# Optimization experiments

Hardware: AMD Instinct MI355X
Metric: run time of the kernel (lower is better)

Reference implementation:

```python
import jax, jax.numpy as jnp
import numpy as np

E = 1024      # embed_dim
H = 16        # num_heads
HD = E // H   # head_dim = 64


def setup_inputs() -> dict:
    key = jax.random.key(0)
    ks = jax.random.split(key, 8)
    T, B, S = 1024, 4, 1024
    return {
        "query": jax.random.normal(ks[0], (T, B, E), jnp.float32),
        "key": jax.random.normal(ks[1], (S, B, E), jnp.float32),
        "value": jax.random.normal(ks[2], (S, B, E), jnp.float32),
        "attn_mask": jax.random.normal(ks[3], (T, S), jnp.float32),
        "key_padding_mask": jax.random.randint(ks[4], (B, S), 0, 2, jnp.int32),
        "in_proj_weight": jax.random.normal(ks[5], (3 * E, E), jnp.float32) * 0.02,
        "in_proj_bias": jnp.zeros((3 * E,), jnp.float32),
        "out_w": jax.random.normal(ks[6], (E, E), jnp.float32) * 0.02,
        "out_b": jnp.zeros((E,), jnp.float32),
    }


def reference(query, key, value, attn_mask, key_padding_mask,
              in_proj_weight, in_proj_bias, out_w, out_b):
    T, B, _ = query.shape
    S = key.shape[0]
    w_q, w_k, w_v = jnp.split(in_proj_weight, 3, axis=0)   # each [E, E]
    b_q, b_k, b_v = jnp.split(in_proj_bias, 3, axis=0)
    q = query @ w_q.T + b_q                                # [T, B, E]
    k = key @ w_k.T + b_k                                  # [S, B, E]
    v = value @ w_v.T + b_v                                # [S, B, E]
    # [len, B, E] -> [B*H, len, HD]
    q = q.reshape(T, B * H, HD).transpose(1, 0, 2) / jnp.sqrt(jnp.float32(HD))
    k = k.reshape(S, B * H, HD).transpose(1, 0, 2)
    v = v.reshape(S, B * H, HD).transpose(1, 0, 2)
    scores = jnp.einsum('bth,bsh->bts', q, k)              # [B*H, T, S]
    scores = scores + attn_mask[None]                      # float additive mask
    pad = key_padding_mask.astype(bool)                    # [B, S]
    pad = jnp.broadcast_to(pad[:, None, None, :], (B, H, 1, S)).reshape(B * H, 1, S)
    scores = jnp.where(pad, -jnp.inf, scores)
    weights = jax.nn.softmax(scores, axis=-1)              # dropout p=0 -> identity
    out = jnp.einsum('bts,bsh->bth', weights, v)           # [B*H, T, HD]
    out = out.transpose(1, 0, 2).reshape(T, B, E)
    out = out @ out_w.T + out_b
    weights_avg = weights.reshape(B, H, T, S).mean(axis=1) # sum/H == mean
    return out, weights_avg
```

## Files before the change

kernel.cpp:

```cpp
#include <hip/hip_runtime.h>
#include <stdint.h>

typedef short bf16x8 __attribute__((ext_vector_type(8)));
typedef float f32x4  __attribute__((ext_vector_type(4)));

#define LOG2E_F 1.4426950408889634f
#define QSCALE_F 0.1803368801111204f

__device__ __forceinline__ unsigned short f2bf(float f) {
    unsigned int u = __float_as_uint(f);
    return (unsigned short)((u + 0x7FFFu + ((u >> 16) & 1u)) >> 16);
}

__device__ __forceinline__ unsigned short f2bfu(float f) {
    return (unsigned short)((__float_as_uint(f) + 0x8000u) >> 16);
}

__device__ __forceinline__ uint4 pack8(float4 a, float4 b) {
    union { unsigned short us[8]; uint4 v; } p;
    p.us[0] = f2bf(a.x); p.us[1] = f2bf(a.y); p.us[2] = f2bf(a.z); p.us[3] = f2bf(a.w);
    p.us[4] = f2bf(b.x); p.us[5] = f2bf(b.y); p.us[6] = f2bf(b.z); p.us[7] = f2bf(b.w);
    return p.v;
}

__global__ __launch_bounds__(256)
void cvt_kernel(const float* __restrict__ q, const float* __restrict__ k,
                const float* __restrict__ v, const float* __restrict__ w,
                const float* __restrict__ ow,
                uint4* __restrict__ Xb, uint4* __restrict__ Wb, uint4* __restrict__ OWb)
{
    const unsigned g = blockIdx.x * 256 + threadIdx.x;
    const float* src;
    uint4* dst;
    if (g < 1572864u) {
        dst = Xb + g;
        if (g < 524288u)        src = q + (size_t)g * 8;
        else if (g < 1048576u)  src = k + (size_t)(g - 524288u) * 8;
        else                    src = v + (size_t)(g - 1048576u) * 8;
    } else if (g < 1966080u) {
        src = w + (size_t)(g - 1572864u) * 8;
        dst = Wb + (g - 1572864u);
    } else {
        src = ow + (size_t)(g - 1966080u) * 8;
        dst = OWb + (g - 1966080u);
    }
    float4 a = *(const float4*)src;
    float4 b = *(const float4*)(src + 4);
    *dst = pack8(a, b);
}

__global__ __launch_bounds__(256)
void mtr_kernel(const float* __restrict__ m, float* __restrict__ mt)
{
    __shared__ float tile[64][65];
    const int bt = (blockIdx.x & 15) << 6;
    const int bs = (blockIdx.x >> 4) << 6;
    const int tx = threadIdx.x & 63;
    const int ty = threadIdx.x >> 6;
#pragma unroll
    for (int i = 0; i < 64; i += 4)
        tile[ty + i][tx] = m[(size_t)(bt + ty + i) * 1024 + bs + tx];
    __syncthreads();
#pragma unroll
    for (int i = 0; i < 64; i += 4) {
        const int s = bs + ty + i;
        mt[(size_t)(s >> 2) * 4096 + (bt + tx) * 4 + (s & 3)] = tile[tx][ty + i];
    }
}

__global__ __launch_bounds__(256)
void qkv_proj_kernel(const unsigned short* __restrict__ Xb, const unsigned short* __restrict__ Wb,
                     const float* __restrict__ bias,
                     unsigned short* __restrict__ Qb, unsigned short* __restrict__ Kb,
                     unsigned short* __restrict__ Vtb)
{
    const int z = blockIdx.z;
    const int j   = blockIdx.x;
    const int xcd = j & 7, idx = j >> 3;
    const int row0 = ((xcd << 2) + (idx >> 3)) * 128;
    const int col0 = (idx & 7) * 128;
    const int wofs = z << 10;

    const unsigned short* A = Xb + (size_t)z * 4194304;
    const unsigned short* B = Wb;

    __shared__ __align__(16) unsigned short As[128 * 72];
    __shared__ __align__(16) unsigned short Bs[128 * 72];

    const int tid  = threadIdx.x;
    const int lane = tid & 63;
    const int wv   = tid >> 6;
    const int wr   = wv >> 1, wc = wv & 1;

    const f32x4 zero4 = {0.f, 0.f, 0.f, 0.f};
    f32x4 acc[4][4];
#pragma unroll
    for (int m = 0; m < 4; ++m)
#pragma unroll
        for (int n = 0; n < 4; ++n) acc[m][n] = zero4;

    const int srow = tid >> 1;
    const int scol = (tid & 1) << 5;
    const int arow = wr * 64 + (lane & 15);
    const int brow = wc * 64 + (lane & 15);
    const int kof  = (lane >> 4) << 3;

    const unsigned short* pa = A + (size_t)(row0 + srow) * 1024 + scol;
    const unsigned short* pb = B + (size_t)(wofs + col0 + srow) * 1024 + scol;
    uint4 ra0 = *(const uint4*)(pa + 0),  ra1 = *(const uint4*)(pa + 8);
    uint4 ra2 = *(const uint4*)(pa + 16), ra3 = *(const uint4*)(pa + 24);
    uint4 rb0 = *(const uint4*)(pb + 0),  rb1 = *(const uint4*)(pb + 8);
    uint4 rb2 = *(const uint4*)(pb + 16), rb3 = *(const uint4*)(pb + 24);

    for (int k0 = 0; k0 < 1024; k0 += 64) {
        __syncthreads();
        *(uint4*)&As[srow * 72 + scol]      = ra0;
        *(uint4*)&As[srow * 72 + scol + 8]  = ra1;
        *(uint4*)&As[srow * 72 + scol + 16] = ra2;
        *(uint4*)&As[srow * 72 + scol + 24] = ra3;
        *(uint4*)&Bs[srow * 72 + scol]      = rb0;
        *(uint4*)&Bs[srow * 72 + scol + 8]  = rb1;
        *(uint4*)&Bs[srow * 72 + scol + 16] = rb2;
        *(uint4*)&Bs[srow * 72 + scol + 24] = rb3;
        __syncthreads();

        if (k0 < 960) {
            pa = A + (size_t)(row0 + srow) * 1024 + k0 + 64 + scol;
            pb = B + (size_t)(wofs + col0 + srow) * 1024 + k0 + 64 + scol;
            ra0 = *(const uint4*)(pa + 0);  ra1 = *(const uint4*)(pa + 8);
            ra2 = *(const uint4*)(pa + 16); ra3 = *(const uint4*)(pa + 24);
            rb0 = *(const uint4*)(pb + 0);  rb1 = *(const uint4*)(pb + 8);
            rb2 = *(const uint4*)(pb + 16); rb3 = *(const uint4*)(pb + 24);
        }

#pragma unroll
        for (int kk = 0; kk < 2; ++kk) {
            bf16x8 af[4], bfr[4];
#pragma unroll
            for (int m = 0; m < 4; ++m)
                af[m] = *(const bf16x8*)&As[(arow + m * 16) * 72 + kk * 32 + kof];
#pragma unroll
            for (int n = 0; n < 4; ++n)
                bfr[n] = *(const bf16x8*)&Bs[(brow + n * 16) * 72 + kk * 32 + kof];
#pragma unroll
            for (int m = 0; m < 4; ++m)
#pragma unroll
                for (int n = 0; n < 4; ++n)
                    acc[m][n] = __builtin_amdgcn_mfma_f32_16x16x32_bf16(af[m], bfr[n], acc[m][n], 0, 0, 0);
        }
    }

    const int ccol = lane & 15;
    const int crow = (lane >> 4) << 2;
#pragma unroll
    for (int n = 0; n < 4; ++n) {
        const int gc   = col0 + wc * 64 + n * 16 + ccol;
        const float bv = bias[wofs + gc];
        const int head = gc >> 6, d = gc & 63;
#pragma unroll
        for (int m = 0; m < 4; ++m) {
#pragma unroll
            for (int r = 0; r < 4; ++r) {
                const int gr = row0 + wr * 64 + m * 16 + crow + r;
                const int t  = gr >> 2, b = gr & 3;
                const int bh = (b << 4) + head;
                float vv = acc[m][n][r] + bv;
                if (z == 0)      Qb [((size_t)bh << 16) + ((size_t)t << 6) + d]  = f2bf(vv * QSCALE_F);
                else if (z == 1) Kb [((size_t)bh << 16) + ((size_t)t << 6) + d]  = f2bf(vv);
                else             Vtb[((size_t)bh << 16) + ((size_t)d << 10) + t] = f2bf(vv);
            }
        }
    }
}

__global__ __launch_bounds__(512)
void flash_kernel(const unsigned short* __restrict__ Qb, const unsigned short* __restrict__ Kb,
                  const unsigned short* __restrict__ Vtb, const float* __restrict__ maskT,
                  const int* __restrict__ padmask,
                  float* __restrict__ rl_buf, unsigned short* __restrict__ attn_out)
{
    const int j   = blockIdx.x;
    const int xcd = j & 7, idx = j >> 3;
    const int bh  = xcd * 8 + (idx >> 3);
    const int t0  = (idx & 7) << 7;
    const int b   = bh >> 4, h = bh & 15;

    __shared__ __align__(16) unsigned short Ks[2][2][64 * 72];
    __shared__ __align__(16) unsigned short Vs[2][2][64 * 72];

    const int tid  = threadIdx.x;
    const int lane = tid & 63;
    const int wv   = tid >> 6;
    const int kof  = (lane >> 4) << 3;
    const int c16  = lane & 15;
    const int g4   = (lane >> 4) << 2;

    const unsigned short* Qbase = Qb  + ((size_t)bh << 16);
    const unsigned short* Kbase = Kb  + ((size_t)bh << 16);
    const unsigned short* Vbase = Vtb + ((size_t)bh << 16);

    bf16x8 qf[2];
#pragma unroll
    for (int kk = 0; kk < 2; ++kk)
        qf[kk] = *(const bf16x8*)(Qbase + ((size_t)(t0 + wv * 16 + c16) << 6) + kk * 32 + kof);

    const bf16x8 ones = {16256, 16256, 16256, 16256, 16256, 16256, 16256, 16256};

    const f32x4 zero4 = {0.f, 0.f, 0.f, 0.f};
    f32x4 acco[4];
#pragma unroll
    for (int nd = 0; nd < 4; ++nd) acco[nd] = zero4;
    f32x4 acc_l = zero4;

    const int srow_st = tid >> 3;
    const int scol_st = (tid & 7) << 3;

    const int bb  = scol_st & 31;
    const int hh  = scol_st & 32;
    const int cL  = hh + ((bb & 15) >> 2) * 8 + (bb >> 4) * 4;
    const int bb4 = bb + 4;
    const int cH  = hh + ((bb4 & 15) >> 2) * 8 + (bb4 >> 4) * 4;

    const int tr2 = t0 + wv * 16 + c16;

    const unsigned short* kp = Kbase + ((size_t)srow_st << 6) + scol_st;
    const unsigned short* vp = Vbase + ((size_t)srow_st << 10) + scol_st;
    uint4 kA = *(const uint4*)kp;
    uint4 kB = *(const uint4*)(kp + 4096);
    uint4 vA = *(const uint4*)vp;
    uint4 vB = *(const uint4*)(vp + 64);

    {
        *(uint4*)&Ks[0][0][srow_st * 72 + scol_st] = kA;
        *(uint4*)&Ks[0][1][srow_st * 72 + scol_st] = kB;
        uint2 lo, hi;
        lo.x = vA.x; lo.y = vA.y; hi.x = vA.z; hi.y = vA.w;
        *(uint2*)&Vs[0][0][srow_st * 72 + cL] = lo;
        *(uint2*)&Vs[0][0][srow_st * 72 + cH] = hi;
        lo.x = vB.x; lo.y = vB.y; hi.x = vB.z; hi.y = vB.w;
        *(uint2*)&Vs[0][1][srow_st * 72 + cL] = lo;
        *(uint2*)&Vs[0][1][srow_st * 72 + cH] = hi;
    }
    kp = Kbase + ((size_t)(128 + srow_st) << 6) + scol_st;
    vp = Vbase + ((size_t)srow_st << 10) + 128 + scol_st;
    kA = *(const uint4*)kp;
    kB = *(const uint4*)(kp + 4096);
    vA = *(const uint4*)vp;
    vB = *(const uint4*)(vp + 64);
    __syncthreads();

    for (int rd = 0; rd < 8; ++rd) {
        const int cur = rd & 1;
        const int s0  = rd << 7;

        if (rd < 7) {
            *(uint4*)&Ks[cur ^ 1][0][srow_st * 72 + scol_st] = kA;
            *(uint4*)&Ks[cur ^ 1][1][srow_st * 72 + scol_st] = kB;
            uint2 lo, hi;
            lo.x = vA.x; lo.y = vA.y; hi.x = vA.z; hi.y = vA.w;
            *(uint2*)&Vs[cur ^ 1][0][srow_st * 72 + cL] = lo;
            *(uint2*)&Vs[cur ^ 1][0][srow_st * 72 + cH] = hi;
            lo.x = vB.x; lo.y = vB.y; hi.x = vB.z; hi.y = vB.w;
            *(uint2*)&Vs[cur ^ 1][1][srow_st * 72 + cL] = lo;
            *(uint2*)&Vs[cur ^ 1][1][srow_st * 72 + cH] = hi;
        }
        if (rd < 6) {
            const int sn = s0 + 256;
            kp = Kbase + ((size_t)(sn + srow_st) << 6) + scol_st;
            vp = Vbase + ((size_t)srow_st << 10) + sn + scol_st;
            kA = *(const uint4*)kp;
            kB = *(const uint4*)(kp + 4096);
            vA = *(const uint4*)vp;
            vB = *(const uint4*)(vp + 64);
        }

        f32x4 accsA[4], accsB[4];
#pragma unroll
        for (int n = 0; n < 4; ++n) { accsA[n] = zero4; accsB[n] = zero4; }
        __builtin_amdgcn_s_setprio(1);
#pragma unroll
        for (int n = 0; n < 4; ++n) {
            bf16x8 kfA0 = *(const bf16x8*)&Ks[cur][0][(n * 16 + c16) * 72 + kof];
            bf16x8 kfA1 = *(const bf16x8*)&Ks[cur][0][(n * 16 + c16) * 72 + 32 + kof];
            accsA[n] = __builtin_amdgcn_mfma_f32_16x16x32_bf16(kfA0, qf[0], accsA[n], 0, 0, 0);
            accsA[n] = __builtin_amdgcn_mfma_f32_16x16x32_bf16(kfA1, qf[1], accsA[n], 0, 0, 0);
            bf16x8 kfB0 = *(const bf16x8*)&Ks[cur][1][(n * 16 + c16) * 72 + kof];
            bf16x8 kfB1 = *(const bf16x8*)&Ks[cur][1][(n * 16 + c16) * 72 + 32 + kof];
            accsB[n] = __builtin_amdgcn_mfma_f32_16x16x32_bf16(kfB0, qf[0], accsB[n], 0, 0, 0);
            accsB[n] = __builtin_amdgcn_mfma_f32_16x16x32_bf16(kfB1, qf[1], accsB[n], 0, 0, 0);
        }
        __builtin_amdgcn_s_setprio(0);

#pragma unroll
        for (int tile = 0; tile < 2; ++tile) {
            const int s0t = s0 + tile * 64;
            f32x4* accs = tile ? accsB : accsA;

            float4 mk[4];
            int4 pd[4];
#pragma unroll
            for (int n = 0; n < 4; ++n) {
                const int srow = s0t + n * 16 + g4;
                pd[n] = *(const int4*)(padmask + (b << 10) + srow);
                mk[n] = *(const float4*)(maskT + (size_t)(srow >> 2) * 4096 + tr2 * 4);
            }

            union { unsigned short us[16]; bf16x8 v[2]; } pk;
#pragma unroll
            for (int n = 0; n < 4; ++n) {
                float x0 = fmaf(mk[n].x, LOG2E_F, accs[n][0]);
                float x1 = fmaf(mk[n].y, LOG2E_F, accs[n][1]);
                float x2 = fmaf(mk[n].z, LOG2E_F, accs[n][2]);
                float x3 = fmaf(mk[n].w, LOG2E_F, accs[n][3]);
                if (pd[n].x) x0 = -1e30f;
                if (pd[n].y) x1 = -1e30f;
                if (pd[n].z) x2 = -1e30f;
                if (pd[n].w) x3 = -1e30f;
                pk.us[n * 4 + 0] = f2bfu(__builtin_amdgcn_exp2f(x0));
                pk.us[n * 4 + 1] = f2bfu(__builtin_amdgcn_exp2f(x1));
                pk.us[n * 4 + 2] = f2bfu(__builtin_amdgcn_exp2f(x2));
                pk.us[n * 4 + 3] = f2bfu(__builtin_amdgcn_exp2f(x3));
            }

            __builtin_amdgcn_s_setprio(1);
#pragma unroll
            for (int hhh = 0; hhh < 2; ++hhh) {
                bf16x8 pf = pk.v[hhh];
#pragma unroll
                for (int nd = 0; nd < 4; ++nd) {
                    bf16x8 vf = *(const bf16x8*)&Vs[cur][tile][(nd * 16 + c16) * 72 + hhh * 32 + kof];
                    acco[nd] = __builtin_amdgcn_mfma_f32_16x16x32_bf16(pf, vf, acco[nd], 0, 0, 0);
                }
                acc_l = __builtin_amdgcn_mfma_f32_16x16x32_bf16(pf, ones, acc_l, 0, 0, 0);
            }
            __builtin_amdgcn_s_setprio(0);
        }

        if (rd < 7) __syncthreads();
    }

#pragma unroll
    for (int r = 0; r < 4; ++r) {
        const int t = t0 + wv * 16 + g4 + r;
        const float rl = 1.0f / acc_l[r];
        if (c16 == 0)
            rl_buf[(bh << 10) + t] = rl;
#pragma unroll
        for (int nd = 0; nd < 4; ++nd) {
            const int d = nd * 16 + c16;
            attn_out[((size_t)t * 4 + b) * 1024 + h * 64 + d] = f2bf(acco[nd][r] * rl);
        }
    }
}

__global__ __launch_bounds__(256)
void wavg_kernel(const unsigned short* __restrict__ Qb, const unsigned short* __restrict__ Kb,
                 const float* __restrict__ attn_mask, const int* __restrict__ padmask,
                 const float* __restrict__ rl_buf, float* __restrict__ wout)
{
    const int j   = blockIdx.x;
    const int xcd = j & 7;
    const int b   = xcd >> 1;
    const int rr  = ((j >> 3) << 1) + (xcd & 1);
    const int t0  = (rr >> 4) << 6;
    const int s0  = (rr & 15) << 6;

    __shared__ __align__(16) unsigned short Qs[2][64 * 72];
    __shared__ __align__(16) unsigned short Ks2[2][64 * 72];

    const int tid  = threadIdx.x;
    const int lane = tid & 63;
    const int wv   = tid >> 6;
    const int wr   = wv >> 1, wc = wv & 1;
    const int kof  = (lane >> 4) << 3;
    const int srow_st = tid >> 2;
    const int scol_st = (tid & 3) << 4;

    const int t_base = t0 + wr * 32 + ((lane >> 4) << 2);
    const int s_base = s0 + wc * 32 + (lane & 15);

    int pad2[2];
#pragma unroll
    for (int nn = 0; nn < 2; ++nn) pad2[nn] = padmask[(b << 10) + s_base + nn * 16];

    float maskv[2][2][4];
#pragma unroll
    for (int mm = 0; mm < 2; ++mm)
#pragma unroll
        for (int r = 0; r < 4; ++r)
#pragma unroll
            for (int nn = 0; nn < 2; ++nn)
                maskv[mm][nn][r] = attn_mask[(size_t)(t_base + mm * 16 + r) * 1024 + s_base + nn * 16] * LOG2E_F;

    float wsum[2][2][4];
#pragma unroll
    for (int mm = 0; mm < 2; ++mm)
#pragma unroll
        for (int nn = 0; nn < 2; ++nn)
#pragma unroll
            for (int r = 0; r < 4; ++r) wsum[mm][nn][r] = 0.f;

    const unsigned short* qsrc = Qb + ((size_t)(t0 + srow_st) << 6) + scol_st;
    const unsigned short* ksrc = Kb + ((size_t)(s0 + srow_st) << 6) + scol_st;
    const size_t bh0 = (size_t)(b << 4) << 16;

    uint4 q0 = *(const uint4*)(qsrc + bh0);
    uint4 q1 = *(const uint4*)(qsrc + bh0 + 8);
    uint4 k0 = *(const uint4*)(ksrc + bh0);
    uint4 k1 = *(const uint4*)(ksrc + bh0 + 8);
    *(uint4*)&Qs[0][srow_st * 72 + scol_st]      = q0;
    *(uint4*)&Qs[0][srow_st * 72 + scol_st + 8]  = q1;
    *(uint4*)&Ks2[0][srow_st * 72 + scol_st]     = k0;
    *(uint4*)&Ks2[0][srow_st * 72 + scol_st + 8] = k1;
    q0 = *(const uint4*)(qsrc + bh0 + 65536);
    q1 = *(const uint4*)(qsrc + bh0 + 65536 + 8);
    k0 = *(const uint4*)(ksrc + bh0 + 65536);
    k1 = *(const uint4*)(ksrc + bh0 + 65536 + 8);
    __syncthreads();

#pragma unroll 2
    for (int h = 0; h < 16; ++h) {
        const int cur = h & 1;
        const int bh  = (b << 4) + h;

        if (h < 15) {
            *(uint4*)&Qs[cur ^ 1][srow_st * 72 + scol_st]      = q0;
            *(uint4*)&Qs[cur ^ 1][srow_st * 72 + scol_st + 8]  = q1;
            *(uint4*)&Ks2[cur ^ 1][srow_st * 72 + scol_st]     = k0;
            *(uint4*)&Ks2[cur ^ 1][srow_st * 72 + scol_st + 8] = k1;
        }
        if (h < 14) {
            const size_t of = bh0 + (size_t)(h + 2) * 65536;
            q0 = *(const uint4*)(qsrc + of);
            q1 = *(const uint4*)(qsrc + of + 8);
            k0 = *(const uint4*)(ksrc + of);
            k1 = *(const uint4*)(ksrc + of + 8);
        }

        float rlv[2][4];
#pragma unroll
        for (int mm = 0; mm < 2; ++mm)
#pragma unroll
            for (int r = 0; r < 4; ++r)
                rlv[mm][r] = rl_buf[(bh << 10) + t_base + mm * 16 + r];

        const f32x4 zero4 = {0.f, 0.f, 0.f, 0.f};
        f32x4 accs[2][2];
#pragma unroll
        for (int mm = 0; mm < 2; ++mm)
#pragma unroll
            for (int nn = 0; nn < 2; ++nn) accs[mm][nn] = zero4;
#pragma unroll
        for (int nn = 0; nn < 2; ++nn) {
            bf16x8 kf0 = *(const bf16x8*)&Ks2[cur][(wc * 32 + nn * 16 + (lane & 15)) * 72 + kof];
            bf16x8 kf1 = *(const bf16x8*)&Ks2[cur][(wc * 32 + nn * 16 + (lane & 15)) * 72 + 32 + kof];
#pragma unroll
            for (int mm = 0; mm < 2; ++mm) {
                bf16x8 qf0 = *(const bf16x8*)&Qs[cur][(wr * 32 + mm * 16 + (lane & 15)) * 72 + kof];
                bf16x8 qf1 = *(const bf16x8*)&Qs[cur][(wr * 32 + mm * 16 + (lane & 15)) * 72 + 32 + kof];
                accs[mm][nn] = __builtin_amdgcn_mfma_f32_16x16x32_bf16(qf0, kf0, accs[mm][nn], 0, 0, 0);
                accs[mm][nn] = __builtin_amdgcn_mfma_f32_16x16x32_bf16(qf1, kf1, accs[mm][nn], 0, 0, 0);
            }
        }
#pragma unroll
        for (int mm = 0; mm < 2; ++mm)
#pragma unroll
            for (int nn = 0; nn < 2; ++nn)
#pragma unroll
                for (int r = 0; r < 4; ++r)
                    if (!pad2[nn]) {
                        float x = accs[mm][nn][r] + maskv[mm][nn][r];
                        wsum[mm][nn][r] += __builtin_amdgcn_exp2f(x) * rlv[mm][r];
                    }

        if (h < 15) __syncthreads();
    }

#pragma unroll
    for (int mm = 0; mm < 2; ++mm)
#pragma unroll
        for (int nn = 0; nn < 2; ++nn)
#pragma unroll
            for (int r = 0; r < 4; ++r)
                wout[((size_t)b << 20) + (size_t)(t_base + mm * 16 + r) * 1024 + s_base + nn * 16]
                    = wsum[mm][nn][r] * 0.0625f;
}

__global__ __launch_bounds__(256)
void out_proj_kernel(const unsigned short* __restrict__ A, const unsigned short* __restrict__ Wb,
                     const float* __restrict__ bias, float* __restrict__ out)
{
    const int j   = blockIdx.x;
    const int xcd = j & 7, idx = j >> 3;
    const int row0 = ((xcd << 2) + (idx >> 3)) * 128;
    const int col0 = (idx & 7) * 128;

    __shared__ __align__(16) unsigned short As[128 * 72];
    __shared__ __align__(16) unsigned short Bs[128 * 72];

    const int tid  = threadIdx.x;
    const int lane = tid & 63;
    const int wv   = tid >> 6;
    const int wr   = wv >> 1, wc = wv & 1;

    const f32x4 zero4 = {0.f, 0.f, 0.f, 0.f};
    f32x4 acc[4][4];
#pragma unroll
    for (int m = 0; m < 4; ++m)
#pragma unroll
        for (int n = 0; n < 4; ++n) acc[m][n] = zero4;

    const int srow = tid >> 1;
    const int scol = (tid & 1) << 5;
    const int arow = wr * 64 + (lane & 15);
    const int brow = wc * 64 + (lane & 15);
    const int kof  = (lane >> 4) << 3;

    const unsigned short* pa = A  + (size_t)(row0 + srow) * 1024 + scol;
    const unsigned short* pb = Wb + (size_t)(col0 + srow) * 1024 + scol;
    uint4 ra0 = *(const uint4*)(pa + 0),  ra1 = *(const uint4*)(pa + 8);
    uint4 ra2 = *(const uint4*)(pa + 16), ra3 = *(const uint4*)(pa + 24);
    uint4 rb0 = *(const uint4*)(pb + 0),  rb1 = *(const uint4*)(pb + 8);
    uint4 rb2 = *(const uint4*)(pb + 16), rb3 = *(const uint4*)(pb + 24);

    for (int k0 = 0; k0 < 1024; k0 += 64) {
        __syncthreads();
        *(uint4*)&As[srow * 72 + scol]      = ra0;
        *(uint4*)&As[srow * 72 + scol + 8]  = ra1;
        *(uint4*)&As[srow * 72 + scol + 16] = ra2;
        *(uint4*)&As[srow * 72 + scol + 24] = ra3;
        *(uint4*)&Bs[srow * 72 + scol]      = rb0;
        *(uint4*)&Bs[srow * 72 + scol + 8]  = rb1;
        *(uint4*)&Bs[srow * 72 + scol + 16] = rb2;
        *(uint4*)&Bs[srow * 72 + scol + 24] = rb3;
        __syncthreads();

        if (k0 < 960) {
            pa = A  + (size_t)(row0 + srow) * 1024 + k0 + 64 + scol;
            pb = Wb + (size_t)(col0 + srow) * 1024 + k0 + 64 + scol;
            ra0 = *(const uint4*)(pa + 0);  ra1 = *(const uint4*)(pa + 8);
            ra2 = *(const uint4*)(pa + 16); ra3 = *(const uint4*)(pa + 24);
            rb0 = *(const uint4*)(pb + 0);  rb1 = *(const uint4*)(pb + 8);
            rb2 = *(const uint4*)(pb + 16); rb3 = *(const uint4*)(pb + 24);
        }

#pragma unroll
        for (int kk = 0; kk < 2; ++kk) {
            bf16x8 af[4], bfr[4];
#pragma unroll
            for (int m = 0; m < 4; ++m)
                af[m] = *(const bf16x8*)&As[(arow + m * 16) * 72 + kk * 32 + kof];
#pragma unroll
            for (int n = 0; n < 4; ++n)
                bfr[n] = *(const bf16x8*)&Bs[(brow + n * 16) * 72 + kk * 32 + kof];
#pragma unroll
            for (int m = 0; m < 4; ++m)
#pragma unroll
                for (int n = 0; n < 4; ++n)
                    acc[m][n] = __builtin_amdgcn_mfma_f32_16x16x32_bf16(af[m], bfr[n], acc[m][n], 0, 0, 0);
        }
    }

    const int ccol = lane & 15;
    const int crow = (lane >> 4) << 2;
#pragma unroll
    for (int n = 0; n < 4; ++n) {
        const int gc   = col0 + wc * 64 + n * 16 + ccol;
        const float bv = bias[gc];
#pragma unroll
        for (int m = 0; m < 4; ++m) {
#pragma unroll
            for (int r = 0; r < 4; ++r) {
                const int gr = row0 + wr * 64 + m * 16 + crow + r;
                out[(size_t)gr * 1024 + gc] = acc[m][n][r] + bv;
            }
        }
    }
}

extern "C" void kernel_launch(void* const* d_in, const int* in_sizes, int n_in,
                              void* d_out, int out_size, void* d_ws, size_t ws_size,
                              hipStream_t stream)
{
    const float* query     = (const float*)d_in[0];
    const float* key       = (const float*)d_in[1];
    const float* value     = (const float*)d_in[2];
    const float* attn_mask = (const float*)d_in[3];
    const int*   padmask   = (const int*)  d_in[4];
    const float* in_proj_w = (const float*)d_in[5];
    const float* in_proj_b = (const float*)d_in[6];
    const float* out_w     = (const float*)d_in[7];
    const float* out_b     = (const float*)d_in[8];

    float* out  = (float*)d_out;
    float* wavg = out + 4194304;

    char* ws = (char*)d_ws;
    unsigned short* Qb     = (unsigned short*)(ws);
    unsigned short* Kb     = (unsigned short*)(ws + 8388608);
    unsigned short* Vtb    = (unsigned short*)(ws + 16777216);
    unsigned short* Xb     = (unsigned short*)(ws + 25165824);
    unsigned short* attn_o = (unsigned short*)(ws + 25165824);
    float*          maskT  = (float*)(ws + 33554432);
    unsigned short* Wb     = (unsigned short*)(ws + 50331648);
    unsigned short* OWb    = (unsigned short*)(ws + 56623104);
    float*          rl_buf = (float*)(ws + 58720256);

    cvt_kernel<<<dim3(8192), 256, 0, stream>>>(query, key, value, in_proj_w, out_w,
                                               (uint4*)Xb, (uint4*)Wb, (uint4*)OWb);
    qkv_proj_kernel<<<dim3(256, 1, 3), 256, 0, stream>>>(Xb, Wb, in_proj_b, Qb, Kb, Vtb);
    mtr_kernel<<<dim3(256), 256, 0, stream>>>(attn_mask, maskT);
    flash_kernel<<<dim3(512), 512, 0, stream>>>(Qb, Kb, Vtb, maskT, padmask,
                                                rl_buf, attn_o);
    wavg_kernel<<<dim3(1024), 256, 0, stream>>>(Qb, Kb, attn_mask, padmask,
                                                rl_buf, wavg);
    out_proj_kernel<<<dim3(256), 256, 0, stream>>>(attn_o, OWb, out_b, out);
}
```

Baseline: 154.7 us.

## Load GEMM tiles directly into LDS via global_load_lds in projection kernels

```diff
diff --git a/kernel.cpp b/kernel.cpp
--- a/kernel.cpp
+++ b/kernel.cpp
@@ -21,6 +21,12 @@
     p.us[0] = f2bf(a.x); p.us[1] = f2bf(a.y); p.us[2] = f2bf(a.z); p.us[3] = f2bf(a.w);
     p.us[4] = f2bf(b.x); p.us[5] = f2bf(b.y); p.us[6] = f2bf(b.z); p.us[7] = f2bf(b.w);
     return p.v;
+}
+
+__device__ __forceinline__ void gload_lds16(const unsigned short* g, unsigned short* l) {
+    __builtin_amdgcn_global_load_lds(
+        (const __attribute__((address_space(1))) void*)g,
+        (__attribute__((address_space(3))) void*)l, 16, 0, 0);
 }
 
 __global__ __launch_bounds__(256)
@@ -84,13 +90,15 @@
     const unsigned short* A = Xb + (size_t)z * 4194304;
     const unsigned short* B = Wb;
 
-    __shared__ __align__(16) unsigned short As[128 * 72];
-    __shared__ __align__(16) unsigned short Bs[128 * 72];
+    __shared__ __align__(16) unsigned short As[128 * 32];
+    __shared__ __align__(16) unsigned short Bs[128 * 32];
 
     const int tid  = threadIdx.x;
     const int lane = tid & 63;
     const int wv   = tid >> 6;
     const int wr   = wv >> 1, wc = wv & 1;
+    const int c16  = lane & 15;
+    const int kof  = (lane >> 4) << 3;
 
     const f32x4 zero4 = {0.f, 0.f, 0.f, 0.f};
     f32x4 acc[4][4];
@@ -99,58 +107,37 @@
 #pragma unroll
         for (int n = 0; n < 4; ++n) acc[m][n] = zero4;
 
-    const int srow = tid >> 1;
-    const int scol = (tid & 1) << 5;
-    const int arow = wr * 64 + (lane & 15);
-    const int brow = wc * 64 + (lane & 15);
-    const int kof  = (lane >> 4) << 3;
-
-    const unsigned short* pa = A + (size_t)(row0 + srow) * 1024 + scol;
-    const unsigned short* pb = B + (size_t)(wofs + col0 + srow) * 1024 + scol;
-    uint4 ra0 = *(const uint4*)(pa + 0),  ra1 = *(const uint4*)(pa + 8);
-    uint4 ra2 = *(const uint4*)(pa + 16), ra3 = *(const uint4*)(pa + 24);
-    uint4 rb0 = *(const uint4*)(pb + 0),  rb1 = *(const uint4*)(pb + 8);
-    uint4 rb2 = *(const uint4*)(pb + 16), rb3 = *(const uint4*)(pb + 24);
-
-    for (int k0 = 0; k0 < 1024; k0 += 64) {
+    const unsigned short* gA = A + (size_t)(row0 + wv * 16 + (lane >> 2)) * 1024 + ((lane & 3) << 3);
+    const unsigned short* gB = B + (size_t)(wofs + col0 + wv * 16 + (lane >> 2)) * 1024 + ((lane & 3) << 3);
+    unsigned short* lA = As + tid * 8;
+    unsigned short* lB = Bs + tid * 8;
+
+    const int arow = wr * 64 + c16;
+    const int brow = wc * 64 + c16;
+
+    for (int k0 = 0; k0 < 1024; k0 += 32) {
         __syncthreads();
-        *(uint4*)&As[srow * 72 + scol]      = ra0;
-        *(uint4*)&As[srow * 72 + scol + 8]  = ra1;
-        *(uint4*)&As[srow * 72 + scol + 16] = ra2;
-        *(uint4*)&As[srow * 72 + scol + 24] = ra3;
-        *(uint4*)&Bs[srow * 72 + scol]      = rb0;
-        *(uint4*)&Bs[srow * 72 + scol + 8]  = rb1;
-        *(uint4*)&Bs[srow * 72 + scol + 16] = rb2;
-        *(uint4*)&Bs[srow * 72 + scol + 24] = rb3;
+        gload_lds16(gA + k0,         lA);
+        gload_lds16(gA + k0 + 65536, lA + 2048);
+        gload_lds16(gB + k0,         lB);
+        gload_lds16(gB + k0 + 65536, lB + 2048);
         __syncthreads();
 
-        if (k0 < 960) {
-            pa = A + (size_t)(row0 + srow) * 1024 + k0 + 64 + scol;
-            pb = B + (size_t)(wofs + col0 + srow) * 1024 + k0 + 64 + scol;
-            ra0 = *(const uint4*)(pa + 0);  ra1 = *(const uint4*)(pa + 8);
-            ra2 = *(const uint4*)(pa + 16); ra3 = *(const uint4*)(pa + 24);
-            rb0 = *(const uint4*)(pb + 0);  rb1 = *(const uint4*)(pb + 8);
-            rb2 = *(const uint4*)(pb + 16); rb3 = *(const uint4*)(pb + 24);
-        }
-
-#pragma unroll
-        for (int kk = 0; kk < 2; ++kk) {
-            bf16x8 af[4], bfr[4];
-#pragma unroll
-            for (int m = 0; m < 4; ++m)
-                af[m] = *(const bf16x8*)&As[(arow + m * 16) * 72 + kk * 32 + kof];
+        bf16x8 af[4], bfr[4];
+#pragma unroll
+        for (int m = 0; m < 4; ++m)
+            af[m] = *(const bf16x8*)&As[(arow + m * 16) * 32 + kof];
+#pragma unroll
+        for (int n = 0; n < 4; ++n)
+            bfr[n] = *(const bf16x8*)&Bs[(brow + n * 16) * 32 + kof];
+#pragma unroll
+        for (int m = 0; m < 4; ++m)
 #pragma unroll
             for (int n = 0; n < 4; ++n)
-                bfr[n] = *(const bf16x8*)&Bs[(brow + n * 16) * 72 + kk * 32 + kof];
-#pragma unroll
-            for (int m = 0; m < 4; ++m)
-#pragma unroll
-                for (int n = 0; n < 4; ++n)
-                    acc[m][n] = __builtin_amdgcn_mfma_f32_16x16x32_bf16(af[m], bfr[n], acc[m][n], 0, 0, 0);
-        }
-    }
-
-    const int ccol = lane & 15;
+                acc[m][n] = __builtin_amdgcn_mfma_f32_16x16x32_bf16(af[m], bfr[n], acc[m][n], 0, 0, 0);
+    }
+
+    const int ccol = c16;
     const int crow = (lane >> 4) << 2;
 #pragma unroll
     for (int n = 0; n < 4; ++n) {
@@ -495,13 +482,15 @@
     const int row0 = ((xcd << 2) + (idx >> 3)) * 128;
     const int col0 = (idx & 7) * 128;
 
-    __shared__ __align__(16) unsigned short As[128 * 72];
-    __shared__ __align__(16) unsigned short Bs[128 * 72];
+    __shared__ __align__(16) unsigned short As[128 * 32];
+    __shared__ __align__(16) unsigned short Bs[128 * 32];
 
     const int tid  = threadIdx.x;
     const int lane = tid & 63;
     const int wv   = tid >> 6;
     const int wr   = wv >> 1, wc = wv & 1;
+    const int c16  = lane & 15;
+    const int kof  = (lane >> 4) << 3;
 
     const f32x4 zero4 = {0.f, 0.f, 0.f, 0.f};
     f32x4 acc[4][4];
@@ -510,58 +499,37 @@
 #pragma unroll
         for (int n = 0; n < 4; ++n) acc[m][n] = zero4;
 
-    const int srow = tid >> 1;
-    const int scol = (tid & 1) << 5;
-    const int arow = wr * 64 + (lane & 15);
-    const int brow = wc * 64 + (lane & 15);
-    const int kof  = (lane >> 4) << 3;
-
-    const unsigned short* pa = A  + (size_t)(row0 + srow) * 1024 + scol;
-    const unsigned short* pb = Wb + (size_t)(col0 + srow) * 1024 + scol;
-    uint4 ra0 = *(const uint4*)(pa + 0),  ra1 = *(const uint4*)(pa + 8);
-    uint4 ra2 = *(const uint4*)(pa + 16), ra3 = *(const uint4*)(pa + 24);
-    uint4 rb0 = *(const uint4*)(pb + 0),  rb1 = *(const uint4*)(pb + 8);
-    uint4 rb2 = *(const uint4*)(pb + 16), rb3 = *(const uint4*)(pb + 24);
-
-    for (int k0 = 0; k0 < 1024; k0 += 64) {
+    const unsigned short* gA = A  + (size_t)(row0 + wv * 16 + (lane >> 2)) * 1024 + ((lane & 3) << 3);
+    const unsigned short* gB = Wb + (size_t)(col0 + wv * 16 + (lane >> 2)) * 1024 + ((lane & 3) << 3);
+    unsigned short* lA = As + tid * 8;
+    unsigned short* lB = Bs + tid * 8;
+
+    const int arow = wr * 64 + c16;
+    const int brow = wc * 64 + c16;
+
+    for (int k0 = 0; k0 < 1024; k0 += 32) {
         __syncthreads();
-        *(uint4*)&As[srow * 72 + scol]      = ra0;
-        *(uint4*)&As[srow * 72 + scol + 8]  = ra1;
-        *(uint4*)&As[srow * 72 + scol + 16] = ra2;
-        *(uint4*)&As[srow * 72 + scol + 24] = ra3;
-        *(uint4*)&Bs[srow * 72 + scol]      = rb0;
-        *(uint4*)&Bs[srow * 72 + scol + 8]  = rb1;
-        *(uint4*)&Bs[srow * 72 + scol + 16] = rb2;
-        *(uint4*)&Bs[srow * 72 + scol + 24] = rb3;
+        gload_lds16(gA + k0,         lA);
+        gload_lds16(gA + k0 + 65536, lA + 2048);
+        gload_lds16(gB + k0,         lB);
+        gload_lds16(gB + k0 + 65536, lB + 2048);
         __syncthreads();
 
-        if (k0 < 960) {
-            pa = A  + (size_t)(row0 + srow) * 1024 + k0 + 64 + scol;
-            pb = Wb + (size_t)(col0 + srow) * 1024 + k0 + 64 + scol;
-            ra0 = *(const uint4*)(pa + 0);  ra1 = *(const uint4*)(pa + 8);
-            ra2 = *(const uint4*)(pa + 16); ra3 = *(const uint4*)(pa + 24);
-            rb0 = *(const uint4*)(pb + 0);  rb1 = *(const uint4*)(pb + 8);
-            rb2 = *(const uint4*)(pb + 16); rb3 = *(const uint4*)(pb + 24);
-        }
-
-#pragma unroll
-        for (int kk = 0; kk < 2; ++kk) {
-            bf16x8 af[4], bfr[4];
-#pragma unroll
-            for (int m = 0; m < 4; ++m)
-                af[m] = *(const bf16x8*)&As[(arow + m * 16) * 72 + kk * 32 + kof];
+        bf16x8 af[4], bfr[4];
+#pragma unroll
+        for (int m = 0; m < 4; ++m)
+            af[m] = *(const bf16x8*)&As[(arow + m * 16) * 32 + kof];
+#pragma unroll
+        for (int n = 0; n < 4; ++n)
+            bfr[n] = *(const bf16x8*)&Bs[(brow + n * 16) * 32 + kof];
+#pragma unroll
+        for (int m = 0; m < 4; ++m)
 #pragma unroll
             for (int n = 0; n < 4; ++n)
-                bfr[n] = *(const bf16x8*)&Bs[(brow + n * 16) * 72 + kk * 32 + kof];
-#pragma unroll
-            for (int m = 0; m < 4; ++m)
-#pragma unroll
-                for (int n = 0; n < 4; ++n)
-                    acc[m][n] = __builtin_amdgcn_mfma_f32_16x16x32_bf16(af[m], bfr[n], acc[m][n], 0, 0, 0);
-        }
-    }
-
-    const int ccol = lane & 15;
+                acc[m][n] = __builtin_amdgcn_mfma_f32_16x16x32_bf16(af[m], bfr[n], acc[m][n], 0, 0, 0);
+    }
+
+    const int ccol = c16;
     const int crow = (lane >> 4) << 2;
 #pragma unroll
     for (int n = 0; n < 4; ++n) {
```

After: 154.0 us. Within noise of the previous version (-0.5%).
